# Performance work log

Measured on AMD Instinct MI355X. Metric: run time of the kernel, lower is better.

Reference implementation:

```python
import jax, jax.numpy as jnp
import numpy as np

B, N, F_IN = 4, 2048, 256
K, D = 4, 64
NEG_SLOPE = 0.2


def setup_inputs() -> dict:
    key = jax.random.key(0)
    k1, k2, k3, k4, k5 = jax.random.split(key, 5)
    x = jax.random.normal(k1, (B, N, F_IN), dtype=jnp.float32)
    adj = jax.random.randint(k2, (B, N, N), 0, 2, dtype=jnp.int32)
    # xavier_uniform-style params
    def xavier(k, shape):
        fan_in, fan_out = shape[-2], shape[-1]
        lim = np.sqrt(6.0 / (fan_in + fan_out))
        return jax.random.uniform(k, shape, jnp.float32, -lim, lim)
    W = xavier(k3, (K, F_IN, D))
    a_src = xavier(k4, (K, D, 1))
    a_dst = xavier(k5, (K, D, 1))
    return {"x": x, "adj": adj, "W": W, "a_src": a_src, "a_dst": a_dst}


def reference(x, adj, W, a_src, a_dst):
    # Wh: (B, K, N, D)
    Wh = jnp.einsum('bnf,kfd->bknd', x, W)
    e_src = jnp.einsum('bknd,kdo->bkno', Wh, a_src)  # (B,K,N,1)
    e_dst = jnp.einsum('bknd,kdo->bkno', Wh, a_dst)  # (B,K,N,1)
    e = e_src + jnp.swapaxes(e_dst, -2, -1)          # (B,K,N,N)
    e = jnp.where(e > 0, e, NEG_SLOPE * e)           # LeakyReLU(0.2)
    # adjacency mask with forced self-loops (adj + I > 0)
    eye = jnp.eye(e.shape[-1], dtype=bool)
    mask = (adj[:, None, :, :] > 0) | eye            # (B,1|K,N,N)
    e = jnp.where(mask, e, -jnp.inf)
    # numerically-stable softmax matching F_module_softmax
    x_max = jnp.max(e, axis=-1, keepdims=True)
    x_max = jnp.where(jnp.isinf(x_max), 0.0, x_max)
    exp_e = jnp.exp(e - x_max)
    exp_e = jnp.where(jnp.isinf(e), 0.0, exp_e)
    alpha = exp_e / (jnp.sum(exp_e, axis=-1, keepdims=True) + 1e-10)
    # dropout is identity in eval mode
    out = jnp.matmul(alpha, Wh)                      # (B,K,N,D)
    # concat heads: (B,N,K*D)
    Bn, Kn, Nn, Dn = out.shape
    return jnp.transpose(out, (0, 2, 1, 3)).reshape(Bn, Nn, Kn * Dn)
```

## Files before the change

kernel.cpp:

```cpp
#include <hip/hip_runtime.h>

#define NB 4
#define NN 2048
#define NF 256
#define NK 4
#define ND 64
#define NEG 0.2f
#define LOG2E 1.4426950408889634f

typedef _Float16 f16;
typedef _Float16 f16x4 __attribute__((ext_vector_type(4)));
typedef _Float16 f16x8 __attribute__((ext_vector_type(8)));
typedef float f32x4 __attribute__((ext_vector_type(4)));

__device__ __forceinline__ int sz2(int d) { return ((d >> 1) ^ (d >> 3)) & 3; }

__global__ __launch_bounds__(256) void k01(
    const float* __restrict__ x,
    const int*   __restrict__ adj,
    const float* __restrict__ Wm,
    const float* __restrict__ a_src,
    const float* __restrict__ a_dst,
    unsigned int* __restrict__ abit,
    f16* __restrict__ wht,
    float* __restrict__ sbuf,
    float* __restrict__ ebuf,
    float* __restrict__ fbuf)
{
    __shared__ f16 wt[64 * 256];

    const int bx  = blockIdx.x;
    const int tid = threadIdx.x;

    if (bx >= 256) {
        const int row = (bx - 256) * 4 + (tid >> 6);
        const int l   = tid & 63;
        const int i   = row & (NN - 1);
        const int* __restrict__ ar = adj + (size_t)row * NN;

        int v[32];
#pragma unroll
        for (int c = 0; c < 32; ++c) v[c] = ar[c * 64 + l];

        unsigned int kx = 0, ky = 0;
#pragma unroll
        for (int c = 0; c < 32; ++c) {
            unsigned long long m = __ballot(v[c] > 0);
            if (l == c) { kx = (unsigned int)m; ky = (unsigned int)(m >> 32); }
        }
        if (l == (i >> 6)) {
            unsigned int sb = 1u << (i & 31);
            if (((i >> 5) & 1) == 0) kx |= sb; else ky |= sb;
        }
        if (l < 32) {
            uint2 kk; kk.x = kx; kk.y = ky;
            *(uint2*)&abit[(size_t)row * 64 + l * 2] = kk;
        }
        return;
    }

    const int gx  = bx & 15;
    const int k   = (bx >> 4) & 3;
    const int b   = bx >> 6;
    const int wv  = tid >> 6;
    const int l   = tid & 63;
    const int q   = l >> 4;
    const int r16 = l & 15;

    for (int fc = 0; fc < 64; ++fc) {
        int f = fc * 4 + wv;
        int d = l;
        wt[d * 256 + (f ^ ((d & 7) << 3))] = (f16)Wm[(k * NF + f) * ND + d];
    }
    __syncthreads();

    const int ncol0 = gx * 128 + wv * 32;
    f32x4 acc[2][4];
#pragma unroll
    for (int nt = 0; nt < 2; ++nt)
#pragma unroll
        for (int dt = 0; dt < 4; ++dt)
            acc[nt][dt] = (f32x4){0.f, 0.f, 0.f, 0.f};

    for (int fs = 0; fs < 16; ++fs) {
        const int f0 = fs * 16 + q * 4;
        f16x4 af[4];
#pragma unroll
        for (int dt = 0; dt < 4; ++dt) {
            int d = dt * 16 + r16;
            af[dt] = *(const f16x4*)&wt[d * 256 + (f0 ^ ((d & 7) << 3))];
        }
#pragma unroll
        for (int nt = 0; nt < 2; ++nt) {
            int n = ncol0 + nt * 16 + r16;
            float4 xv = *(const float4*)&x[((size_t)(b * NN + n)) * NF + f0];
            f16x4 bf = {(f16)xv.x, (f16)xv.y, (f16)xv.z, (f16)xv.w};
#pragma unroll
            for (int dt = 0; dt < 4; ++dt)
                acc[nt][dt] = __builtin_amdgcn_mfma_f32_16x16x16f16(
                    af[dt], bf, acc[nt][dt], 0, 0, 0);
        }
    }

    float asv[4][4], adv[4][4];
#pragma unroll
    for (int dt = 0; dt < 4; ++dt)
#pragma unroll
        for (int rr = 0; rr < 4; ++rr) {
            int d = dt * 16 + q * 4 + rr;
            asv[dt][rr] = a_src[k * ND + d];
            adv[dt][rr] = a_dst[k * ND + d];
        }

    const int jt = gx * 4 + wv;
    f16* __restrict__ tile = wht + ((size_t)(b * NK + k) * 64 + jt) * 2048;
    const int qj = r16 >> 2, ee = r16 & 3;

#pragma unroll
    for (int nt = 0; nt < 2; ++nt) {
        int n = ncol0 + nt * 16 + r16;
        float sp = 0.f, tp = 0.f;
#pragma unroll
        for (int dt = 0; dt < 4; ++dt)
#pragma unroll
            for (int rr = 0; rr < 4; ++rr) {
                float v = acc[nt][dt][rr];
                int d = dt * 16 + q * 4 + rr;
                tile[d * 32 + ((qj ^ sz2(d)) << 3) + nt * 4 + ee] = (f16)v;
                sp += v * asv[dt][rr];
                tp += v * adv[dt][rr];
            }
        sp += __shfl_xor(sp, 16);
        sp += __shfl_xor(sp, 32);
        tp += __shfl_xor(tp, 16);
        tp += __shfl_xor(tp, 32);
        if (q == 0) {
            int idx = (b * NK + k) * NN + n;
            sbuf[idx] = sp;
            ebuf[idx] = __builtin_exp2f(tp * LOG2E);
            fbuf[idx] = __builtin_exp2f(0.2f * LOG2E * tp);
        }
    }
}

__global__ __launch_bounds__(512) void k2_attn(
    const unsigned int* __restrict__ abit,
    const f16* __restrict__ wht,
    const float* __restrict__ sbuf,
    const float* __restrict__ ebuf,
    const float* __restrict__ fbuf,
    float* __restrict__ out)
{
    const int i0  = blockIdx.x * 64;
    const int k   = blockIdx.y;
    const int b   = blockIdx.z;
    const int tid = threadIdx.x;
    const int w   = tid >> 6;
    const int c   = w >> 2;
    const int rw  = w & 3;
    const int l   = tid & 63;
    const int q   = l >> 4;
    const int r16 = l & 15;
    const int iglob = i0 + rw * 16 + r16;

    __shared__ char pool[49664];
    float* el   = (float*)(pool + 32768);
    float* fl   = (float*)(pool + 40960);
    float* dden = (float*)(pool + 49152);

    {
        const float* eb = ebuf + (b * NK + k) * NN;
        const float* fb = fbuf + (b * NK + k) * NN;
        *(float4*)&el[tid * 4] = *(const float4*)&eb[tid * 4];
        *(float4*)&fl[tid * 4] = *(const float4*)&fb[tid * 4];
    }

    const float s  = sbuf[(b * NK + k) * NN + iglob];
    const float Af = __builtin_exp2f(0.8f * LOG2E * fminf(s, 0.f));
    const float Bf = __builtin_exp2f(-0.8f * LOG2E * fmaxf(s, 0.f));
    const char* gtiles = (const char*)(wht + (size_t)(b * NK + k) * 64 * 2048);
    const unsigned int* __restrict__ abrow =
        abit + (size_t)(b * NN + iglob) * 64 + c * 32;

    float denom = 0.f;
    f32x4 acc[4];
#pragma unroll
    for (int dt = 0; dt < 4; ++dt) acc[dt] = (f32x4){0.f, 0.f, 0.f, 0.f};

#define STAGE8(bb, it)                                                         \
    do {                                                                       \
        const char* gsrc = gtiles + (size_t)(c * 1024 + (it) * 64) * 128 +     \
                           (tid & 255) * 16;                                   \
        char* ldst = pool + c * 16384 + (bb) * 8192 + (w & 3) * 1024;          \
        __builtin_amdgcn_global_load_lds(                                      \
            (const __attribute__((address_space(1))) void*)gsrc,               \
            (__attribute__((address_space(3))) void*)ldst, 16, 0, 0);          \
        __builtin_amdgcn_global_load_lds(                                      \
            (const __attribute__((address_space(1))) void*)(gsrc + 4096),      \
            (__attribute__((address_space(3))) void*)(ldst + 4096), 16, 0, 0); \
    } while (0)

    STAGE8(0, 0);
    uint2 ab = *(const uint2*)abrow;

    for (int it = 0; it < 16; ++it) {
        __syncthreads();
        uint2 ab_n = ab;
        if (it < 15) {
            STAGE8((it + 1) & 1, it + 1);
            ab_n = *(const uint2*)(abrow + (it + 1) * 2);
        }
        const char* lb0 = pool + c * 16384 + (it & 1) * 8192;
#pragma unroll
        for (int h = 0; h < 2; ++h) {
            const unsigned int bits = h ? ab.y : ab.x;
            const unsigned int bs = bits >> (q * 4);
            const int tb = c * 1024 + it * 64 + h * 32;
            float4 e0 = *(const float4*)&el[tb + q * 4];
            float4 e1 = *(const float4*)&el[tb + 16 + q * 4];
            float4 f0 = *(const float4*)&fl[tb + q * 4];
            float4 f1 = *(const float4*)&fl[tb + 16 + q * 4];
            float ea[4] = {e0.x, e0.y, e0.z, e0.w};
            float eb[4] = {e1.x, e1.y, e1.z, e1.w};
            float fa[4] = {f0.x, f0.y, f0.z, f0.w};
            float fb[4] = {f1.x, f1.y, f1.z, f1.w};
            float w0[4], w1[4];
#pragma unroll
            for (int e = 0; e < 4; ++e) {
                float wa = fmaxf(Af * ea[e], Bf * fa[e]);
                w0[e] = (bs & (1u << e)) ? wa : 0.f;
                float wb = fmaxf(Af * eb[e], Bf * fb[e]);
                w1[e] = (bs & (1u << (16 + e))) ? wb : 0.f;
            }
            denom += ((w0[0] + w0[1]) + (w0[2] + w0[3])) +
                     ((w1[0] + w1[1]) + (w1[2] + w1[3]));
            f16x4 pa0 = {(f16)w0[0], (f16)w0[1], (f16)w0[2], (f16)w0[3]};
            f16x4 pa1 = {(f16)w1[0], (f16)w1[1], (f16)w1[2], (f16)w1[3]};
            const char* lb = lb0 + h * 4096;
#pragma unroll
            for (int dt = 0; dt < 4; ++dt) {
                int d = dt * 16 + r16;
                f16x8 v8 = *(const f16x8*)(lb + d * 64 + ((q ^ sz2(d)) << 4));
                f16x4 bf0 = __builtin_shufflevector(v8, v8, 0, 1, 2, 3);
                f16x4 bf1 = __builtin_shufflevector(v8, v8, 4, 5, 6, 7);
                acc[dt] = __builtin_amdgcn_mfma_f32_16x16x16f16(pa0, bf0,
                                                                acc[dt], 0, 0, 0);
                acc[dt] = __builtin_amdgcn_mfma_f32_16x16x16f16(pa1, bf1,
                                                                acc[dt], 0, 0, 0);
            }
        }
        ab = ab_n;
    }
#undef STAGE8

    denom += __shfl_xor(denom, 16);
    denom += __shfl_xor(denom, 32);

    __syncthreads();
    float* stash = (float*)pool;
    if (c == 1) {
#pragma unroll
        for (int dt = 0; dt < 4; ++dt)
            *(f32x4*)&stash[(rw * 4 + dt) * 256 + l * 4] = acc[dt];
    }
    if (l < 16) dden[c * 64 + rw * 16 + l] = denom;
    __syncthreads();

    if (c == 0) {
#pragma unroll
        for (int dt = 0; dt < 4; ++dt)
            acc[dt] += *(const f32x4*)&stash[(rw * 4 + dt) * 256 + l * 4];
#pragma unroll
        for (int rr = 0; rr < 4; ++rr) {
            int irow = q * 4 + rr;
            float dd = dden[rw * 16 + irow] + dden[64 + rw * 16 + irow];
            float inv = 1.f / (dd + 1e-10f);
#pragma unroll
            for (int dt = 0; dt < 4; ++dt)
                out[((size_t)(b * NN) + i0 + rw * 16 + irow) * (NK * ND) +
                    k * ND + dt * 16 + r16] = acc[dt][rr] * inv;
        }
    }
}

extern "C" void kernel_launch(void* const* d_in, const int* in_sizes, int n_in,
                              void* d_out, int out_size, void* d_ws, size_t ws_size,
                              hipStream_t stream) {
    const float* x     = (const float*)d_in[0];
    const int*   adj   = (const int*)d_in[1];
    const float* Wm    = (const float*)d_in[2];
    const float* a_src = (const float*)d_in[3];
    const float* a_dst = (const float*)d_in[4];
    float* out = (float*)d_out;

    char* ws = (char*)d_ws;
    f16*   wht  = (f16*)ws;
    float* sbuf = (float*)(ws + (4u << 20));
    float* ebuf = (float*)(ws + (4u << 20) + (128u << 10));
    float* fbuf = (float*)(ws + (4u << 20) + (256u << 10));
    unsigned int* abit = (unsigned int*)(ws + (4u << 20) + (384u << 10));

    k01<<<dim3(256 + NB * NN / 4), 256, 0, stream>>>(
        x, adj, Wm, a_src, a_dst, abit, wht, sbuf, ebuf, fbuf);
    k2_attn<<<dim3(NN / 64, NK, NB), 512, 0, stream>>>(
        abit, wht, sbuf, ebuf, fbuf, out);
}
```

Baseline: 50.45 us.

## Triple-buffer attention tiles, prefetch adjacency bits, use 16x16x32 MFMA

Turns the double-buffered LDS staging of Wh tiles into a three-stage ring with explicit vmcnt waits and raw s_barrier. Only the needed loads must land before each iteration, which hides more global latency. All sixteen adjacency bit words are loaded into registers up front, and the pair of 16x16x16 MFMAs per d-tile becomes one gfx950 16x16x32 f16 MFMA. LDS use grows to about 66KB per block and register pressure rises from the abx array and full unroll, which may cut occupancy despite the launch-bounds hint.

```diff
diff --git a/kernel.cpp b/kernel.cpp
--- a/kernel.cpp
+++ b/kernel.cpp
@@ -143,7 +143,7 @@
     }
 }
 
-__global__ __launch_bounds__(512) void k2_attn(
+__global__ __launch_bounds__(512, 4) void k2_attn(
     const unsigned int* __restrict__ abit,
     const f16* __restrict__ wht,
     const float* __restrict__ sbuf,
@@ -163,10 +163,16 @@
     const int r16 = l & 15;
     const int iglob = i0 + rw * 16 + r16;
 
-    __shared__ char pool[49664];
-    float* el   = (float*)(pool + 32768);
-    float* fl   = (float*)(pool + 40960);
-    float* dden = (float*)(pool + 49152);
+    __shared__ char pool[66048];
+    float* el   = (float*)(pool + 49152);
+    float* fl   = (float*)(pool + 57344);
+    float* dden = (float*)(pool + 65536);
+
+    const unsigned int* __restrict__ abrow =
+        abit + (size_t)(b * NN + iglob) * 64 + c * 32;
+    uint2 abx[16];
+#pragma unroll
+    for (int it = 0; it < 16; ++it) abx[it] = *(const uint2*)(abrow + it * 2);
 
     {
         const float* eb = ebuf + (b * NK + k) * NN;
@@ -179,8 +185,6 @@
     const float Af = __builtin_exp2f(0.8f * LOG2E * fminf(s, 0.f));
     const float Bf = __builtin_exp2f(-0.8f * LOG2E * fmaxf(s, 0.f));
     const char* gtiles = (const char*)(wht + (size_t)(b * NK + k) * 64 * 2048);
-    const unsigned int* __restrict__ abrow =
-        abit + (size_t)(b * NN + iglob) * 64 + c * 32;
 
     float denom = 0.f;
     f32x4 acc[4];
@@ -191,7 +195,7 @@
     do {                                                                       \
         const char* gsrc = gtiles + (size_t)(c * 1024 + (it) * 64) * 128 +     \
                            (tid & 255) * 16;                                   \
-        char* ldst = pool + c * 16384 + (bb) * 8192 + (w & 3) * 1024;          \
+        char* ldst = pool + c * 24576 + (bb) * 8192 + (w & 3) * 1024;          \
         __builtin_amdgcn_global_load_lds(                                      \
             (const __attribute__((address_space(1))) void*)gsrc,               \
             (__attribute__((address_space(3))) void*)ldst, 16, 0, 0);          \
@@ -201,16 +205,21 @@
     } while (0)
 
     STAGE8(0, 0);
-    uint2 ab = *(const uint2*)abrow;
-
+    STAGE8(1, 1);
+
+#pragma unroll
     for (int it = 0; it < 16; ++it) {
-        __syncthreads();
-        uint2 ab_n = ab;
-        if (it < 15) {
-            STAGE8((it + 1) & 1, it + 1);
-            ab_n = *(const uint2*)(abrow + (it + 1) * 2);
-        }
-        const char* lb0 = pool + c * 16384 + (it & 1) * 8192;
+        if (it < 15)
+            asm volatile("s_waitcnt vmcnt(2) lgkmcnt(0)" ::: "memory");
+        else
+            asm volatile("s_waitcnt vmcnt(0) lgkmcnt(0)" ::: "memory");
+        __builtin_amdgcn_sched_barrier(0);
+        __builtin_amdgcn_s_barrier();
+        __builtin_amdgcn_sched_barrier(0);
+        if (it < 14) STAGE8((it + 2) % 3, it + 2);
+
+        const char* lb0 = pool + c * 24576 + (it % 3) * 8192;
+        const uint2 ab = abx[it];
 #pragma unroll
         for (int h = 0; h < 2; ++h) {
             const unsigned int bits = h ? ab.y : ab.x;
@@ -234,22 +243,17 @@
             }
             denom += ((w0[0] + w0[1]) + (w0[2] + w0[3])) +
                      ((w1[0] + w1[1]) + (w1[2] + w1[3]));
-            f16x4 pa0 = {(f16)w0[0], (f16)w0[1], (f16)w0[2], (f16)w0[3]};
-            f16x4 pa1 = {(f16)w1[0], (f16)w1[1], (f16)w1[2], (f16)w1[3]};
+            f16x8 pa = {(f16)w0[0], (f16)w0[1], (f16)w0[2], (f16)w0[3],
+                        (f16)w1[0], (f16)w1[1], (f16)w1[2], (f16)w1[3]};
             const char* lb = lb0 + h * 4096;
 #pragma unroll
             for (int dt = 0; dt < 4; ++dt) {
                 int d = dt * 16 + r16;
                 f16x8 v8 = *(const f16x8*)(lb + d * 64 + ((q ^ sz2(d)) << 4));
-                f16x4 bf0 = __builtin_shufflevector(v8, v8, 0, 1, 2, 3);
-                f16x4 bf1 = __builtin_shufflevector(v8, v8, 4, 5, 6, 7);
-                acc[dt] = __builtin_amdgcn_mfma_f32_16x16x16f16(pa0, bf0,
-                                                                acc[dt], 0, 0, 0);
-                acc[dt] = __builtin_amdgcn_mfma_f32_16x16x16f16(pa1, bf1,
-                                                                acc[dt], 0, 0, 0);
+                acc[dt] = __builtin_amdgcn_mfma_f32_16x16x32_f16(
+                    pa, v8, acc[dt], 0, 0, 0);
             }
         }
-        ab = ab_n;
     }
 #undef STAGE8
 
```

New measurement: 47.76 us. -5.3%, faster.
